# Kernel tuning notes

Measured on AMD Instinct MI355X. Metric: run time of the kernel, lower is better.

## Reference

```python
import jax, jax.numpy as jnp
import numpy as np

B, S, H, DH = 4, 1024, 8, 64
D = H * DH
CLIP_K = 5
NUM_RPR = 2 * CLIP_K + 1  # 11


def setup_inputs() -> dict:
    key = jax.random.key(0)
    ks = jax.random.split(key, 12)
    w_scale = 0.01  # truncated_normal stddev approx
    inp = {
        'q': jax.random.normal(ks[0], (B, S, D), jnp.float32),
        'k': jax.random.normal(ks[1], (B, S, D), jnp.float32),
        'v': jax.random.normal(ks[2], (B, S, D), jnp.float32),
        'rpr_matrix': jax.random.randint(ks[3], (S, S), 0, NUM_RPR, jnp.int32),
        'wq_kernel': jax.random.normal(ks[4], (D, D), jnp.float32) * w_scale,
        'wq_bias': jnp.zeros((D,), jnp.float32),
        'wk_kernel': jax.random.normal(ks[5], (D, D), jnp.float32) * w_scale,
        'wk_bias': jnp.zeros((D,), jnp.float32),
        'wv_kernel': jax.random.normal(ks[6], (D, D), jnp.float32) * w_scale,
        'wv_bias': jnp.zeros((D,), jnp.float32),
        'krpr': jax.random.normal(ks[7], (NUM_RPR, DH), jnp.float32),
    }
    return inp


def reference(q, k, v, rpr_matrix, wq_kernel, wq_bias, wk_kernel, wk_bias,
              wv_kernel, wv_bias, krpr):
    b, s, d = q.shape
    dh = krpr.shape[-1]
    h = d // dh

    def proj(x, w, bias):
        # [B,S,D] -> [B,H,S,DH]
        y = x.reshape(-1, d) @ w + bias
        return y.reshape(b, s, h, dh).transpose(0, 2, 1, 3)

    qh = proj(q, wq_kernel, wq_bias)
    kh = proj(k, wk_kernel, wk_bias)
    vh = proj(v, wv_kernel, wv_bias)

    # standard QK^T scores
    scores = jnp.einsum('bhqd,bhkd->bhqk', qh, kh)
    # RPR key bias: gather per-relative-position key embeddings (note: original
    # code uses krpr for BOTH the key-side and value-side RPR; vrpr is unused)
    alpha = krpr[rpr_matrix]  # [Sq, Sk, DH]
    scores = scores + jnp.einsum('bhqd,qkd->bhqk', qh, alpha)
    scores = scores / jnp.sqrt(jnp.float32(dh))

    probs = jax.nn.softmax(scores, axis=-1)

    ctx = jnp.einsum('bhqk,bhkd->bhqd', probs, vh)
    ctx = ctx + jnp.einsum('bhqk,qkd->bhqd', probs, alpha)

    # [B,H,S,DH] -> [B,S,D]
    return ctx.transpose(0, 2, 1, 3).reshape(b, s, d)
```

## Files before the change

kernel.cpp:

```cpp
#include <hip/hip_runtime.h>

typedef unsigned short u16;
typedef unsigned int u32;
typedef __attribute__((ext_vector_type(8))) short short8;
typedef __attribute__((ext_vector_type(4))) float f32x4;

__device__ __forceinline__ float bf2f(u16 v) {
  return __uint_as_float(((u32)v) << 16);
}
__device__ __forceinline__ u16 f2bf(float f) {
  u32 u = __float_as_uint(f);
  return (u16)((u + 0x7fffu + ((u >> 16) & 1u)) >> 16);
}
__device__ __forceinline__ u32 pk2(float lo, float hi) {
  return (u32)f2bf(lo) | ((u32)f2bf(hi) << 16);
}

__device__ __forceinline__ float ld1in(const void* p, size_t i, bool f32) {
  return f32 ? ((const float*)p)[i] : bf2f(((const u16*)p)[i]);
}
__device__ __forceinline__ float4 ld4in(const void* p, size_t i, bool f32) {
  if (f32) return *(const float4*)((const float*)p + i);
  ushort4 u = *(const ushort4*)((const u16*)p + i);
  return make_float4(bf2f(u.x), bf2f(u.y), bf2f(u.z), bf2f(u.w));
}

__device__ __forceinline__ float4 ld4ws(const u16* p, size_t i) {
  ushort4 u = *(const ushort4*)(p + i);
  return make_float4(bf2f(u.x), bf2f(u.y), bf2f(u.z), bf2f(u.w));
}
__device__ __forceinline__ uint4 ld8ws_pk(const u16* p, size_t i) {
  return *(const uint4*)(p + i);
}


__global__ void rpr_detect_kernel(const u16* __restrict__ q, int* __restrict__ flag) {
  __shared__ int cnt[256];
  int t = threadIdx.x, c = 0;
  for (int i = t; i < 8192; i += 256) {
    unsigned e = (q[i] >> 7) & 0xff;
    c += (e >= 0xC0) ? 1 : 0;
  }
  cnt[t] = c;
  __syncthreads();
  if (t == 0) {
    int s = 0;
    for (int i = 0; i < 256; ++i) s += cnt[i];
    *flag = (s > 128) ? 1 : 0;
  }
}

template <typename WT>
__global__ __launch_bounds__(256, 2) void rpr_proj_mfma(
    const void* __restrict__ xq, const void* __restrict__ xk, const void* __restrict__ xv,
    const void* __restrict__ wqp, const void* __restrict__ wkp, const void* __restrict__ wvp,
    const void* __restrict__ bqp, const void* __restrict__ bkp, const void* __restrict__ bvp,
    WT* __restrict__ ws, const int* __restrict__ flagp) {
  const bool f32 = (*flagp != 0);
  const int z = blockIdx.z;
  const void* __restrict__ X = (z == 0) ? xq : (z == 1) ? xk : xv;
  const void* __restrict__ W = (z == 0) ? wqp : (z == 1) ? wkp : wvp;
  const void* __restrict__ Bb = (z == 0) ? bqp : (z == 1) ? bkp : bvp;
  WT* __restrict__ O = ws + (size_t)z * (4096u * 512u);

  __shared__ u32 as32[2][64][20];
  __shared__ u32 bs32[2][64][20];

  const int t = threadIdx.x;
  const int wvi = t >> 6, lane = t & 63;
  const int quad = lane >> 4, col = lane & 15;
  const int m0 = blockIdx.y * 64, n0 = blockIdx.x * 64;
  const int am = t >> 2, akc = t & 3;
  const int bkx = t & 15, bnx = (t >> 4) * 4;

  f32x4 acc[4] = {{0.f, 0.f, 0.f, 0.f}, {0.f, 0.f, 0.f, 0.f},
                  {0.f, 0.f, 0.f, 0.f}, {0.f, 0.f, 0.f, 0.f}};

  auto loadA = [&](int k0, uint4& ra) {
    if (!f32) {
      ra = *(const uint4*)((const u16*)X + (size_t)(m0 + am) * 512 + k0 + akc * 8);
    } else {
      const float* xf = (const float*)X + (size_t)(m0 + am) * 512 + k0 + akc * 8;
      float4 a = *(const float4*)xf, b = *(const float4*)(xf + 4);
      ra.x = pk2(a.x, a.y); ra.y = pk2(a.z, a.w);
      ra.z = pk2(b.x, b.y); ra.w = pk2(b.z, b.w);
    }
  };
  auto loadB = [&](int k0, uint4& rb) {
    if (!f32) {
      const u16* w0 = (const u16*)W + (size_t)(k0 + 2 * bkx) * 512 + n0 + bnx;
      ushort4 r0 = *(const ushort4*)w0;
      ushort4 r1 = *(const ushort4*)(w0 + 512);
      rb.x = (u32)r0.x | ((u32)r1.x << 16);
      rb.y = (u32)r0.y | ((u32)r1.y << 16);
      rb.z = (u32)r0.z | ((u32)r1.z << 16);
      rb.w = (u32)r0.w | ((u32)r1.w << 16);
    } else {
      float4 r0 = ld4in(W, (size_t)(k0 + 2 * bkx) * 512 + n0 + bnx, true);
      float4 r1 = ld4in(W, (size_t)(k0 + 2 * bkx + 1) * 512 + n0 + bnx, true);
      rb.x = pk2(r0.x, r1.x);
      rb.y = pk2(r0.y, r1.y);
      rb.z = pk2(r0.z, r1.z);
      rb.w = pk2(r0.w, r1.w);
    }
  };

  {
    uint4 ra, rb;
    loadA(0, ra);
    loadB(0, rb);
    *(uint4*)&as32[0][am][akc * 4] = ra;
    bs32[0][bnx + 0][bkx] = rb.x;
    bs32[0][bnx + 1][bkx] = rb.y;
    bs32[0][bnx + 2][bkx] = rb.z;
    bs32[0][bnx + 3][bkx] = rb.w;
  }
  __syncthreads();

  for (int it = 0; it < 16; ++it) {
    const int cur = it & 1;
    uint4 ra, rb;
    if (it < 15) {
      loadA((it + 1) * 32, ra);
      loadB((it + 1) * 32, rb);
    }
    short8 aF = *(const short8*)((const u16*)&as32[cur][wvi * 16 + col][0] + quad * 8);
#pragma unroll
    for (int c = 0; c < 4; ++c) {
      short8 bF = *(const short8*)((const u16*)&bs32[cur][c * 16 + col][0] + quad * 8);
      acc[c] = __builtin_amdgcn_mfma_f32_16x16x32_bf16(aF, bF, acc[c], 0, 0, 0);
    }
    if (it < 15) {
      *(uint4*)&as32[1 - cur][am][akc * 4] = ra;
      bs32[1 - cur][bnx + 0][bkx] = rb.x;
      bs32[1 - cur][bnx + 1][bkx] = rb.y;
      bs32[1 - cur][bnx + 2][bkx] = rb.z;
      bs32[1 - cur][bnx + 3][bkx] = rb.w;
    }
    __syncthreads();
  }

  const int h = blockIdx.x;
#pragma unroll
  for (int c = 0; c < 4; ++c) {
    float bias = ld1in(Bb, (size_t)(n0 + c * 16 + col), f32);
#pragma unroll
    for (int reg = 0; reg < 4; ++reg) {
      int m = m0 + wvi * 16 + quad * 4 + reg;
      int bb = m >> 10, s = m & 1023;
      O[((size_t)((bb * 8 + h) * 1024 + s)) * 64 + c * 16 + col] =
          f2bf(acc[c][reg] + bias);
    }
  }
}

template <typename WT>
__global__ __launch_bounds__(256, 2) void rpr_attn_mfma(
    const WT* __restrict__ qkv, const int* __restrict__ rpr,
    const void* __restrict__ krpr, void* __restrict__ out,
    const int* __restrict__ flagp) {
  const bool f32 = (*flagp != 0);
  const int bh = blockIdx.y, q0 = blockIdx.x * 64;
  const int b = bh >> 3, h = bh & 7;
  const WT* __restrict__ qh = qkv + (size_t)bh * 65536;
  const WT* __restrict__ kh = qkv + (size_t)(32 + bh) * 65536;
  const WT* __restrict__ vh = qkv + (size_t)(64 + bh) * 65536;

  __shared__ u16 qs[64][72];
  __shared__ u16 ks[2][64][72];
  __shared__ u32 vs32[2][64][36];
  __shared__ u16 ps[4][16][72];
  __shared__ float krl[11][64];
  __shared__ float qrpr[64][12];

  const int t = threadIdx.x;
  const int wvi = t >> 6, lane = t & 63;
  const int quad = lane >> 4, col = lane & 15;
  const int sr = t >> 2, sc4 = (t & 3) * 16;
  const int kp = t & 31, dg = (t >> 5) * 8;

  for (int i = t; i < 704; i += 256)
    krl[i >> 6][i & 63] = f32 ? ((const float*)krpr)[i] : bf2f(((const u16*)krpr)[i]);
  {
    size_t base = (size_t)(q0 + sr) * 64 + sc4;
    *(uint4*)&qs[sr][sc4] = ld8ws_pk(qh, base);
    *(uint4*)&qs[sr][sc4 + 8] = ld8ws_pk(qh, base + 8);
  }
  {
    size_t kb = (size_t)sr * 64 + sc4;
    *(uint4*)&ks[0][sr][sc4] = ld8ws_pk(kh, kb);
    *(uint4*)&ks[0][sr][sc4 + 8] = ld8ws_pk(kh, kb + 8);
    size_t vb = (size_t)(2 * kp) * 64 + dg;
    uint4 va = ld8ws_pk(vh, vb), vbb = ld8ws_pk(vh, vb + 64);
    vs32[0][dg + 0][kp] = (va.x & 0xffffu) | (vbb.x << 16);
    vs32[0][dg + 1][kp] = (va.x >> 16) | (vbb.x & 0xffff0000u);
    vs32[0][dg + 2][kp] = (va.y & 0xffffu) | (vbb.y << 16);
    vs32[0][dg + 3][kp] = (va.y >> 16) | (vbb.y & 0xffff0000u);
    vs32[0][dg + 4][kp] = (va.z & 0xffffu) | (vbb.z << 16);
    vs32[0][dg + 5][kp] = (va.z >> 16) | (vbb.z & 0xffff0000u);
    vs32[0][dg + 6][kp] = (va.w & 0xffffu) | (vbb.w << 16);
    vs32[0][dg + 7][kp] = (va.w >> 16) | (vbb.w & 0xffff0000u);
  }
  __syncthreads();
  {
    int r = t >> 2, rb = t & 3;
    float d0 = 0.f, d1 = 0.f, d2 = 0.f;
    for (int d = 0; d < 64; ++d) {
      float qv = bf2f(qs[r][d]);
      d0 = fmaf(qv, krl[rb][d], d0);
      d1 = fmaf(qv, krl[rb + 4][d], d1);
      if (rb < 3) d2 = fmaf(qv, krl[rb + 8][d], d2);
    }
    qrpr[r][rb] = d0;
    qrpr[r][rb + 4] = d1;
    if (rb < 3) qrpr[r][rb + 8] = d2;
  }
  short8 qA0, qA1;
  {
    const u16* qrow = &qs[wvi * 16 + col][0];
    qA0 = *(const short8*)(qrow + quad * 8);
    qA1 = *(const short8*)(qrow + 32 + quad * 8);
  }
  __syncthreads();

  float l_part[4] = {0.f, 0.f, 0.f, 0.f};
  float bins[4][11] = {};
  f32x4 ctx[4] = {{0.f, 0.f, 0.f, 0.f}, {0.f, 0.f, 0.f, 0.f},
                  {0.f, 0.f, 0.f, 0.f}, {0.f, 0.f, 0.f, 0.f}};

  for (int kt = 0; kt < 16; ++kt) {
    const int cur = kt & 1;
    uint4 pk0, pk1, pva, pvb;
    if (kt < 15) {
      size_t kb = (size_t)((kt + 1) * 64 + sr) * 64 + sc4;
      pk0 = ld8ws_pk(kh, kb);
      pk1 = ld8ws_pk(kh, kb + 8);
      size_t vb = (size_t)((kt + 1) * 64 + 2 * kp) * 64 + dg;
      pva = ld8ws_pk(vh, vb);
      pvb = ld8ws_pk(vh, vb + 64);
    }
    int rid[4][4];
    {
      const int* rbase =
          rpr + (size_t)(q0 + wvi * 16 + quad * 4) * 1024 + kt * 64 + col;
#pragma unroll
      for (int reg = 0; reg < 4; ++reg)
#pragma unroll
        for (int c = 0; c < 4; ++c) rid[c][reg] = rbase[reg * 1024 + c * 16];
    }
    f32x4 sc[4];
#pragma unroll
    for (int c = 0; c < 4; ++c) {
      const u16* kb = &ks[cur][c * 16 + col][0];
      short8 kB0 = *(const short8*)(kb + quad * 8);
      short8 kB1 = *(const short8*)(kb + 32 + quad * 8);
      f32x4 a = {0.f, 0.f, 0.f, 0.f};
      a = __builtin_amdgcn_mfma_f32_16x16x32_bf16(qA0, kB0, a, 0, 0, 0);
      a = __builtin_amdgcn_mfma_f32_16x16x32_bf16(qA1, kB1, a, 0, 0, 0);
      sc[c] = a;
    }
#pragma unroll
    for (int c = 0; c < 4; ++c) {
#pragma unroll
      for (int reg = 0; reg < 4; ++reg) {
        int row = wvi * 16 + quad * 4 + reg;
        float p = __expf((sc[c][reg] + qrpr[row][rid[c][reg]]) * 0.125f);
        l_part[reg] += p;
#pragma unroll
        for (int r = 0; r < 11; ++r) bins[reg][r] += (rid[c][reg] == r) ? p : 0.f;
        ps[wvi][quad * 4 + reg][c * 16 + col] = f2bf(p);
      }
    }
    __syncthreads();

    short8 pA0, pA1;
    {
      const u16* prow = &ps[wvi][col][0];
      pA0 = *(const short8*)(prow + quad * 8);
      pA1 = *(const short8*)(prow + 32 + quad * 8);
    }
#pragma unroll
    for (int c = 0; c < 4; ++c) {
      const u16* vrow = (const u16*)&vs32[cur][c * 16 + col][0];
      short8 vB0 = *(const short8*)(vrow + quad * 8);
      short8 vB1 = *(const short8*)(vrow + 32 + quad * 8);
      ctx[c] = __builtin_amdgcn_mfma_f32_16x16x32_bf16(pA0, vB0, ctx[c], 0, 0, 0);
      ctx[c] = __builtin_amdgcn_mfma_f32_16x16x32_bf16(pA1, vB1, ctx[c], 0, 0, 0);
    }
    if (kt < 15) {
      *(uint4*)&ks[1 - cur][sr][sc4] = pk0;
      *(uint4*)&ks[1 - cur][sr][sc4 + 8] = pk1;
      vs32[1 - cur][dg + 0][kp] = (pva.x & 0xffffu) | (pvb.x << 16);
      vs32[1 - cur][dg + 1][kp] = (pva.x >> 16) | (pvb.x & 0xffff0000u);
      vs32[1 - cur][dg + 2][kp] = (pva.y & 0xffffu) | (pvb.y << 16);
      vs32[1 - cur][dg + 3][kp] = (pva.y >> 16) | (pvb.y & 0xffff0000u);
      vs32[1 - cur][dg + 4][kp] = (pva.z & 0xffffu) | (pvb.z << 16);
      vs32[1 - cur][dg + 5][kp] = (pva.z >> 16) | (pvb.z & 0xffff0000u);
      vs32[1 - cur][dg + 6][kp] = (pva.w & 0xffffu) | (pvb.w << 16);
      vs32[1 - cur][dg + 7][kp] = (pva.w >> 16) | (pvb.w & 0xffff0000u);
    }
    __syncthreads();
  }

#pragma unroll
  for (int off = 1; off < 16; off <<= 1) {
#pragma unroll
    for (int reg = 0; reg < 4; ++reg) {
      l_part[reg] += __shfl_xor(l_part[reg], off);
#pragma unroll
      for (int r = 0; r < 11; ++r) bins[reg][r] += __shfl_xor(bins[reg][r], off);
    }
  }
#pragma unroll
  for (int reg = 0; reg < 4; ++reg) {
    int row = wvi * 16 + quad * 4 + reg;
    float inv = 1.f / l_part[reg];
#pragma unroll
    for (int c = 0; c < 4; ++c) {
      float v = ctx[c][reg];
#pragma unroll
      for (int r = 0; r < 11; ++r) v = fmaf(bins[reg][r], krl[r][c * 16 + col], v);
      size_t oidx = (size_t)(b * 1024 + q0 + row) * 512 + h * 64 + c * 16 + col;
      if (f32) ((float*)out)[oidx] = v * inv;
      else ((u16*)out)[oidx] = f2bf(v * inv);
    }
  }
}

extern "C" void kernel_launch(void* const* d_in, const int* in_sizes, int n_in,
                              void* d_out, int out_size, void* d_ws, size_t ws_size,
                              hipStream_t stream) {
  const void* q = d_in[0];
  const void* k = d_in[1];
  const void* v = d_in[2];
  const int* rpr = (const int*)d_in[3];
  const void* wq = d_in[4];
  const void* bq = d_in[5];
  const void* wk = d_in[6];
  const void* bk = d_in[7];
  const void* wv = d_in[8];
  const void* bv = d_in[9];
  const void* krpr = d_in[10];

  int* flag = (int*)d_ws;
  u16* ws = (u16*)((char*)d_ws + 1024);

  rpr_detect_kernel<<<1, 256, 0, stream>>>((const u16*)q, flag);
  rpr_proj_mfma<u16><<<dim3(8, 64, 3), 256, 0, stream>>>(
      q, k, v, wq, wk, wv, bq, bk, bv, ws, flag);
  rpr_attn_mfma<u16><<<dim3(16, 32), 256, 0, stream>>>(
      ws, rpr, krpr, d_out, flag);
}
```

Measured before the change: 190.9 us.

## Fold softmax scale into exp2, pack P stores, fdot2 RPR binning, permute V rows

Folds the 1/sqrt(dh)*log2(e) scale into qrpr and uses raw v_exp_f32 with an fma in place of __expf. The RPR-bin accumulation becomes packed f16 fdot2 with bitmask selectors instead of 11 compare-selects per element. P is converted with hardware packed bf16 conversion and stored as 8-byte chunks in a permuted column order, with V rows loaded in a matching permuted order so the PV product still lines up. One __syncthreads after the P store is removed, relying on each wave reading only its own ps slice. The costs are f16 rounding of probabilities inside the bin sums and a dependence on the V/P permutation being exactly consistent.

```diff
diff --git a/kernel.cpp b/kernel.cpp
--- a/kernel.cpp
+++ b/kernel.cpp
@@ -4,6 +4,7 @@
 typedef unsigned int u32;
 typedef __attribute__((ext_vector_type(8))) short short8;
 typedef __attribute__((ext_vector_type(4))) float f32x4;
+typedef _Float16 f16x2 __attribute__((ext_vector_type(2)));
 
 __device__ __forceinline__ float bf2f(u16 v) {
   return __uint_as_float(((u32)v) << 16);
@@ -169,7 +170,7 @@
   __shared__ u16 qs[64][72];
   __shared__ u16 ks[2][64][72];
   __shared__ u32 vs32[2][64][36];
-  __shared__ u16 ps[4][16][72];
+  __shared__ alignas(16) u16 ps[4][16][72];
   __shared__ float krl[11][64];
   __shared__ float qrpr[64][12];
 
@@ -178,6 +179,7 @@
   const int quad = lane >> 4, col = lane & 15;
   const int sr = t >> 2, sc4 = (t & 3) * 16;
   const int kp = t & 31, dg = (t >> 5) * 8;
+  const int vr0 = (kp & 1) * 32 + (kp >> 1);
 
   for (int i = t; i < 704; i += 256)
     krl[i >> 6][i & 63] = f32 ? ((const float*)krpr)[i] : bf2f(((const u16*)krpr)[i]);
@@ -190,8 +192,8 @@
     size_t kb = (size_t)sr * 64 + sc4;
     *(uint4*)&ks[0][sr][sc4] = ld8ws_pk(kh, kb);
     *(uint4*)&ks[0][sr][sc4 + 8] = ld8ws_pk(kh, kb + 8);
-    size_t vb = (size_t)(2 * kp) * 64 + dg;
-    uint4 va = ld8ws_pk(vh, vb), vbb = ld8ws_pk(vh, vb + 64);
+    size_t vb = (size_t)vr0 * 64 + dg;
+    uint4 va = ld8ws_pk(vh, vb), vbb = ld8ws_pk(vh, vb + 1024);
     vs32[0][dg + 0][kp] = (va.x & 0xffffu) | (vbb.x << 16);
     vs32[0][dg + 1][kp] = (va.x >> 16) | (vbb.x & 0xffff0000u);
     vs32[0][dg + 2][kp] = (va.y & 0xffffu) | (vbb.y << 16);
@@ -203,6 +205,7 @@
   }
   __syncthreads();
   {
+    const float SC = 0.18033688011112042f;
     int r = t >> 2, rb = t & 3;
     float d0 = 0.f, d1 = 0.f, d2 = 0.f;
     for (int d = 0; d < 64; ++d) {
@@ -211,9 +214,9 @@
       d1 = fmaf(qv, krl[rb + 4][d], d1);
       if (rb < 3) d2 = fmaf(qv, krl[rb + 8][d], d2);
     }
-    qrpr[r][rb] = d0;
-    qrpr[r][rb + 4] = d1;
-    if (rb < 3) qrpr[r][rb + 8] = d2;
+    qrpr[r][rb] = d0 * SC;
+    qrpr[r][rb + 4] = d1 * SC;
+    if (rb < 3) qrpr[r][rb + 8] = d2 * SC;
   }
   short8 qA0, qA1;
   {
@@ -235,9 +238,9 @@
       size_t kb = (size_t)((kt + 1) * 64 + sr) * 64 + sc4;
       pk0 = ld8ws_pk(kh, kb);
       pk1 = ld8ws_pk(kh, kb + 8);
-      size_t vb = (size_t)((kt + 1) * 64 + 2 * kp) * 64 + dg;
+      size_t vb = (size_t)((kt + 1) * 64 + vr0) * 64 + dg;
       pva = ld8ws_pk(vh, vb);
-      pvb = ld8ws_pk(vh, vb + 64);
+      pvb = ld8ws_pk(vh, vb + 1024);
     }
     int rid[4][4];
     {
@@ -260,18 +263,43 @@
       sc[c] = a;
     }
 #pragma unroll
-    for (int c = 0; c < 4; ++c) {
-#pragma unroll
-      for (int reg = 0; reg < 4; ++reg) {
-        int row = wvi * 16 + quad * 4 + reg;
-        float p = __expf((sc[c][reg] + qrpr[row][rid[c][reg]]) * 0.125f);
-        l_part[reg] += p;
-#pragma unroll
-        for (int r = 0; r < 11; ++r) bins[reg][r] += (rid[c][reg] == r) ? p : 0.f;
-        ps[wvi][quad * 4 + reg][c * 16 + col] = f2bf(p);
+    for (int reg = 0; reg < 4; ++reg) {
+      const int row = wvi * 16 + quad * 4 + reg;
+      float p4[4];
+#pragma unroll
+      for (int c = 0; c < 4; ++c) {
+        float x = fmaf(sc[c][reg], 0.18033688011112042f, qrpr[row][rid[c][reg]]);
+        float pe;
+        asm("v_exp_f32 %0, %1" : "=v"(pe) : "v"(x));
+        p4[c] = pe;
+        l_part[reg] += pe;
       }
-    }
-    __syncthreads();
+#if __has_builtin(__builtin_amdgcn_fdot2) && __has_builtin(__builtin_amdgcn_cvt_pkrtz)
+      f16x2 ph01 = __builtin_bit_cast(f16x2, __builtin_amdgcn_cvt_pkrtz(p4[0], p4[1]));
+      f16x2 ph23 = __builtin_bit_cast(f16x2, __builtin_amdgcn_cvt_pkrtz(p4[2], p4[3]));
+      u32 m01 = (1u << (u32)rid[0][reg]) | (0x10000u << (u32)rid[1][reg]);
+      u32 m23 = (1u << (u32)rid[2][reg]) | (0x10000u << (u32)rid[3][reg]);
+#pragma unroll
+      for (int r = 0; r < 11; ++r) {
+        u32 s01 = ((m01 >> r) & 0x00010001u) * 0x3C00u;
+        u32 s23 = ((m23 >> r) & 0x00010001u) * 0x3C00u;
+        bins[reg][r] = __builtin_amdgcn_fdot2(ph01, __builtin_bit_cast(f16x2, s01),
+                                              bins[reg][r], false);
+        bins[reg][r] = __builtin_amdgcn_fdot2(ph23, __builtin_bit_cast(f16x2, s23),
+                                              bins[reg][r], false);
+      }
+#else
+#pragma unroll
+      for (int c = 0; c < 4; ++c)
+#pragma unroll
+        for (int r = 0; r < 11; ++r)
+          bins[reg][r] += (rid[c][reg] == r) ? p4[c] : 0.f;
+#endif
+      u32 plo, phi;
+      asm("v_cvt_pk_bf16_f32 %0, %1, %2" : "=v"(plo) : "v"(p4[0]), "v"(p4[1]));
+      asm("v_cvt_pk_bf16_f32 %0, %1, %2" : "=v"(phi) : "v"(p4[2]), "v"(p4[3]));
+      *(uint2*)&ps[wvi][quad * 4 + reg][col * 4] = make_uint2(plo, phi);
+    }
 
     short8 pA0, pA1;
     {
```

Result: faster. 181.5 us (-4.9%).

## Split key tile across two wave groups in attention, with fp16 dot2 binning and exp2

Applied to the files above, without the earlier changes.

The attention block grows to 512 threads, and each of the two wave halves handles 32 of the 64 keys per tile. The partial context, row sums and RPR bins are then merged through shared memory at the end. The softmax scale is folded into an exp2 constant and applied to the precomputed q·krpr table. Per-bin accumulation now uses packed fp16 dot2 with bitmask selectors, and the per-wave P buffer reuses the Q staging area. The aim is more parallelism and less VALU work per key, at the cost of an extra reduction step and lower-precision (fp16 RTZ) bin sums.

```diff
diff --git a/kernel.cpp b/kernel.cpp
--- a/kernel.cpp
+++ b/kernel.cpp
@@ -4,6 +4,7 @@
 typedef unsigned int u32;
 typedef __attribute__((ext_vector_type(8))) short short8;
 typedef __attribute__((ext_vector_type(4))) float f32x4;
+typedef _Float16 f16x2 __attribute__((ext_vector_type(2)));
 
 __device__ __forceinline__ float bf2f(u16 v) {
   return __uint_as_float(((u32)v) << 16);
@@ -25,29 +26,23 @@
   return make_float4(bf2f(u.x), bf2f(u.y), bf2f(u.z), bf2f(u.w));
 }
 
-__device__ __forceinline__ float4 ld4ws(const u16* p, size_t i) {
-  ushort4 u = *(const ushort4*)(p + i);
-  return make_float4(bf2f(u.x), bf2f(u.y), bf2f(u.z), bf2f(u.w));
-}
 __device__ __forceinline__ uint4 ld8ws_pk(const u16* p, size_t i) {
   return *(const uint4*)(p + i);
 }
 
 
 __global__ void rpr_detect_kernel(const u16* __restrict__ q, int* __restrict__ flag) {
-  __shared__ int cnt[256];
+  __shared__ int cnt4[4];
   int t = threadIdx.x, c = 0;
   for (int i = t; i < 8192; i += 256) {
     unsigned e = (q[i] >> 7) & 0xff;
     c += (e >= 0xC0) ? 1 : 0;
   }
-  cnt[t] = c;
-  __syncthreads();
-  if (t == 0) {
-    int s = 0;
-    for (int i = 0; i < 256; ++i) s += cnt[i];
-    *flag = (s > 128) ? 1 : 0;
-  }
+#pragma unroll
+  for (int off = 1; off < 64; off <<= 1) c += __shfl_xor(c, off);
+  if ((t & 63) == 0) cnt4[t >> 6] = c;
+  __syncthreads();
+  if (t == 0) *flag = (cnt4[0] + cnt4[1] + cnt4[2] + cnt4[3] > 128) ? 1 : 0;
 }
 
 template <typename WT>
@@ -155,7 +150,7 @@
 }
 
 template <typename WT>
-__global__ __launch_bounds__(256, 2) void rpr_attn_mfma(
+__global__ __launch_bounds__(512, 4) void rpr_attn_mfma(
     const WT* __restrict__ qkv, const int* __restrict__ rpr,
     const void* __restrict__ krpr, void* __restrict__ out,
     const int* __restrict__ flagp) {
@@ -166,58 +161,51 @@
   const WT* __restrict__ kh = qkv + (size_t)(32 + bh) * 65536;
   const WT* __restrict__ vh = qkv + (size_t)(64 + bh) * 65536;
 
-  __shared__ u16 qs[64][72];
   __shared__ u16 ks[2][64][72];
   __shared__ u32 vs32[2][64][36];
-  __shared__ u16 ps[4][16][72];
+  __shared__ u16 qps[64][72];
   __shared__ float krl[11][64];
   __shared__ float qrpr[64][12];
 
   const int t = threadIdx.x;
-  const int wvi = t >> 6, lane = t & 63;
+  const int w = t >> 6, lane = t & 63;
   const int quad = lane >> 4, col = lane & 15;
-  const int sr = t >> 2, sc4 = (t & 3) * 16;
-  const int kp = t & 31, dg = (t >> 5) * 8;
-
-  for (int i = t; i < 704; i += 256)
+  const int qg = w & 3, h2 = w >> 2;
+  const int sr = t >> 3, sc = (t & 7) * 8;
+  const int kp = t & 31, dgv = (t >> 5) * 4;
+  const int vr0 = (kp & 15) + (kp >> 4) * 32;
+
+  u16* __restrict__ psw = &qps[0][0] + w * (16 * 36);
+
+  for (int i = t; i < 704; i += 512)
     krl[i >> 6][i & 63] = f32 ? ((const float*)krpr)[i] : bf2f(((const u16*)krpr)[i]);
+  *(uint4*)&qps[sr][sc] = ld8ws_pk(qh, (size_t)(q0 + sr) * 64 + sc);
+  *(uint4*)&ks[0][sr][sc] = ld8ws_pk(kh, (size_t)sr * 64 + sc);
   {
-    size_t base = (size_t)(q0 + sr) * 64 + sc4;
-    *(uint4*)&qs[sr][sc4] = ld8ws_pk(qh, base);
-    *(uint4*)&qs[sr][sc4 + 8] = ld8ws_pk(qh, base + 8);
-  }
+    const u16* vp = vh + (size_t)vr0 * 64 + dgv;
+    uint2 va = *(const uint2*)vp;
+    uint2 vbb = *(const uint2*)(vp + 1024);
+    vs32[0][dgv + 0][kp] = (va.x & 0xffffu) | (vbb.x << 16);
+    vs32[0][dgv + 1][kp] = (va.x >> 16) | (vbb.x & 0xffff0000u);
+    vs32[0][dgv + 2][kp] = (va.y & 0xffffu) | (vbb.y << 16);
+    vs32[0][dgv + 3][kp] = (va.y >> 16) | (vbb.y & 0xffff0000u);
+  }
+  __syncthreads();
   {
-    size_t kb = (size_t)sr * 64 + sc4;
-    *(uint4*)&ks[0][sr][sc4] = ld8ws_pk(kh, kb);
-    *(uint4*)&ks[0][sr][sc4 + 8] = ld8ws_pk(kh, kb + 8);
-    size_t vb = (size_t)(2 * kp) * 64 + dg;
-    uint4 va = ld8ws_pk(vh, vb), vbb = ld8ws_pk(vh, vb + 64);
-    vs32[0][dg + 0][kp] = (va.x & 0xffffu) | (vbb.x << 16);
-    vs32[0][dg + 1][kp] = (va.x >> 16) | (vbb.x & 0xffff0000u);
-    vs32[0][dg + 2][kp] = (va.y & 0xffffu) | (vbb.y << 16);
-    vs32[0][dg + 3][kp] = (va.y >> 16) | (vbb.y & 0xffff0000u);
-    vs32[0][dg + 4][kp] = (va.z & 0xffffu) | (vbb.z << 16);
-    vs32[0][dg + 5][kp] = (va.z >> 16) | (vbb.z & 0xffff0000u);
-    vs32[0][dg + 6][kp] = (va.w & 0xffffu) | (vbb.w << 16);
-    vs32[0][dg + 7][kp] = (va.w >> 16) | (vbb.w & 0xffff0000u);
-  }
-  __syncthreads();
-  {
-    int r = t >> 2, rb = t & 3;
-    float d0 = 0.f, d1 = 0.f, d2 = 0.f;
+    const float SC = 0.18033688011112042f;
+    int r = t >> 3, j = t & 7;
+    float d0 = 0.f, d1 = 0.f;
     for (int d = 0; d < 64; ++d) {
-      float qv = bf2f(qs[r][d]);
-      d0 = fmaf(qv, krl[rb][d], d0);
-      d1 = fmaf(qv, krl[rb + 4][d], d1);
-      if (rb < 3) d2 = fmaf(qv, krl[rb + 8][d], d2);
-    }
-    qrpr[r][rb] = d0;
-    qrpr[r][rb + 4] = d1;
-    if (rb < 3) qrpr[r][rb + 8] = d2;
+      float qv = bf2f(qps[r][d]);
+      d0 = fmaf(qv, krl[j][d], d0);
+      if (j < 3) d1 = fmaf(qv, krl[j + 8][d], d1);
+    }
+    qrpr[r][j] = d0 * SC;
+    if (j < 3) qrpr[r][j + 8] = d1 * SC;
   }
   short8 qA0, qA1;
   {
-    const u16* qrow = &qs[wvi * 16 + col][0];
+    const u16* qrow = &qps[qg * 16 + col][0];
     qA0 = *(const short8*)(qrow + quad * 8);
     qA1 = *(const short8*)(qrow + 32 + quad * 8);
   }
@@ -230,99 +218,129 @@
 
   for (int kt = 0; kt < 16; ++kt) {
     const int cur = kt & 1;
-    uint4 pk0, pk1, pva, pvb;
+    uint4 pk;
+    uint2 pva, pvb;
     if (kt < 15) {
-      size_t kb = (size_t)((kt + 1) * 64 + sr) * 64 + sc4;
-      pk0 = ld8ws_pk(kh, kb);
-      pk1 = ld8ws_pk(kh, kb + 8);
-      size_t vb = (size_t)((kt + 1) * 64 + 2 * kp) * 64 + dg;
-      pva = ld8ws_pk(vh, vb);
-      pvb = ld8ws_pk(vh, vb + 64);
-    }
-    int rid[4][4];
+      pk = ld8ws_pk(kh, (size_t)((kt + 1) * 64 + sr) * 64 + sc);
+      const u16* vp = vh + (size_t)((kt + 1) * 64 + vr0) * 64 + dgv;
+      pva = *(const uint2*)vp;
+      pvb = *(const uint2*)(vp + 1024);
+    }
+    int rid[2][4];
     {
       const int* rbase =
-          rpr + (size_t)(q0 + wvi * 16 + quad * 4) * 1024 + kt * 64 + col;
+          rpr + (size_t)(q0 + qg * 16 + quad * 4) * 1024 + kt * 64 + h2 * 32 + col;
 #pragma unroll
       for (int reg = 0; reg < 4; ++reg)
 #pragma unroll
-        for (int c = 0; c < 4; ++c) rid[c][reg] = rbase[reg * 1024 + c * 16];
-    }
-    f32x4 sc[4];
-#pragma unroll
-    for (int c = 0; c < 4; ++c) {
-      const u16* kb = &ks[cur][c * 16 + col][0];
+        for (int c = 0; c < 2; ++c) rid[c][reg] = rbase[reg * 1024 + c * 16];
+    }
+    f32x4 sc2[2];
+#pragma unroll
+    for (int c = 0; c < 2; ++c) {
+      const u16* kb = &ks[cur][(2 * h2 + c) * 16 + col][0];
       short8 kB0 = *(const short8*)(kb + quad * 8);
       short8 kB1 = *(const short8*)(kb + 32 + quad * 8);
       f32x4 a = {0.f, 0.f, 0.f, 0.f};
       a = __builtin_amdgcn_mfma_f32_16x16x32_bf16(qA0, kB0, a, 0, 0, 0);
       a = __builtin_amdgcn_mfma_f32_16x16x32_bf16(qA1, kB1, a, 0, 0, 0);
-      sc[c] = a;
-    }
+      sc2[c] = a;
+    }
+#pragma unroll
+    for (int reg = 0; reg < 4; ++reg) {
+      const int row = qg * 16 + quad * 4 + reg;
+      float p2[2];
+#pragma unroll
+      for (int c = 0; c < 2; ++c) {
+        float x = fmaf(sc2[c][reg], 0.18033688011112042f, qrpr[row][rid[c][reg]]);
+        float pe;
+        asm("v_exp_f32 %0, %1" : "=v"(pe) : "v"(x));
+        p2[c] = pe;
+        l_part[reg] += pe;
+      }
+      f16x2 ph = __builtin_bit_cast(f16x2, __builtin_amdgcn_cvt_pkrtz(p2[0], p2[1]));
+      u32 m01 = (1u << (u32)rid[0][reg]) | (0x10000u << (u32)rid[1][reg]);
+#pragma unroll
+      for (int r = 0; r < 11; ++r) {
+        u32 s01 = ((m01 >> r) & 0x00010001u) * 0x3C00u;
+        bins[reg][r] = __builtin_amdgcn_fdot2(ph, __builtin_bit_cast(f16x2, s01),
+                                              bins[reg][r], false);
+      }
+      u32 pw;
+      asm("v_cvt_pk_bf16_f32 %0, %1, %2" : "=v"(pw) : "v"(p2[0]), "v"(p2[1]));
+      *(u32*)(psw + (quad * 4 + reg) * 36 + col * 2) = pw;
+    }
+
+    short8 pA = *(const short8*)(psw + col * 36 + quad * 8);
 #pragma unroll
     for (int c = 0; c < 4; ++c) {
+      const u16* vrow = (const u16*)&vs32[cur][c * 16 + col][0] + h2 * 32 + quad * 8;
+      short8 vB = *(const short8*)vrow;
+      ctx[c] = __builtin_amdgcn_mfma_f32_16x16x32_bf16(pA, vB, ctx[c], 0, 0, 0);
+    }
+    if (kt < 15) {
+      *(uint4*)&ks[1 - cur][sr][sc] = pk;
+      vs32[1 - cur][dgv + 0][kp] = (pva.x & 0xffffu) | (pvb.x << 16);
+      vs32[1 - cur][dgv + 1][kp] = (pva.x >> 16) | (pvb.x & 0xffff0000u);
+      vs32[1 - cur][dgv + 2][kp] = (pva.y & 0xffffu) | (pvb.y << 16);
+      vs32[1 - cur][dgv + 3][kp] = (pva.y >> 16) | (pvb.y & 0xffff0000u);
+    }
+    __syncthreads();
+  }
+
+#pragma unroll
+  for (int off = 1; off < 16; off <<= 1) {
+#pragma unroll
+    for (int reg = 0; reg < 4; ++reg) {
+      l_part[reg] += __shfl_xor(l_part[reg], off);
+#pragma unroll
+      for (int r = 0; r < 11; ++r) bins[reg][r] += __shfl_xor(bins[reg][r], off);
+    }
+  }
+
+  float* __restrict__ cm = (float*)&ks[0][0][0];
+  float* __restrict__ lb = (float*)&vs32[0][0][0];
+  if (h2 == 1) {
+    float* cp = cm + ((size_t)(qg * 64 + lane)) * 16;
+#pragma unroll
+    for (int c = 0; c < 4; ++c)
+#pragma unroll
+      for (int reg = 0; reg < 4; ++reg) cp[c * 4 + reg] = ctx[c][reg];
+    if (col == 0) {
+      float* lp = lb + (size_t)((qg * 4 + quad) * 4) * 12;
 #pragma unroll
       for (int reg = 0; reg < 4; ++reg) {
-        int row = wvi * 16 + quad * 4 + reg;
-        float p = __expf((sc[c][reg] + qrpr[row][rid[c][reg]]) * 0.125f);
-        l_part[reg] += p;
-#pragma unroll
-        for (int r = 0; r < 11; ++r) bins[reg][r] += (rid[c][reg] == r) ? p : 0.f;
-        ps[wvi][quad * 4 + reg][c * 16 + col] = f2bf(p);
+        lp[reg * 12] = l_part[reg];
+#pragma unroll
+        for (int r = 0; r < 11; ++r) lp[reg * 12 + 1 + r] = bins[reg][r];
       }
     }
-    __syncthreads();
-
-    short8 pA0, pA1;
-    {
-      const u16* prow = &ps[wvi][col][0];
-      pA0 = *(const short8*)(prow + quad * 8);
-      pA1 = *(const short8*)(prow + 32 + quad * 8);
-    }
-#pragma unroll
-    for (int c = 0; c < 4; ++c) {
-      const u16* vrow = (const u16*)&vs32[cur][c * 16 + col][0];
-      short8 vB0 = *(const short8*)(vrow + quad * 8);
-      short8 vB1 = *(const short8*)(vrow + 32 + quad * 8);
-      ctx[c] = __builtin_amdgcn_mfma_f32_16x16x32_bf16(pA0, vB0, ctx[c], 0, 0, 0);
-      ctx[c] = __builtin_amdgcn_mfma_f32_16x16x32_bf16(pA1, vB1, ctx[c], 0, 0, 0);
-    }
-    if (kt < 15) {
-      *(uint4*)&ks[1 - cur][sr][sc4] = pk0;
-      *(uint4*)&ks[1 - cur][sr][sc4 + 8] = pk1;
-      vs32[1 - cur][dg + 0][kp] = (pva.x & 0xffffu) | (pvb.x << 16);
-      vs32[1 - cur][dg + 1][kp] = (pva.x >> 16) | (pvb.x & 0xffff0000u);
-      vs32[1 - cur][dg + 2][kp] = (pva.y & 0xffffu) | (pvb.y << 16);
-      vs32[1 - cur][dg + 3][kp] = (pva.y >> 16) | (pvb.y & 0xffff0000u);
-      vs32[1 - cur][dg + 4][kp] = (pva.z & 0xffffu) | (pvb.z << 16);
-      vs32[1 - cur][dg + 5][kp] = (pva.z >> 16) | (pvb.z & 0xffff0000u);
-      vs32[1 - cur][dg + 6][kp] = (pva.w & 0xffffu) | (pvb.w << 16);
-      vs32[1 - cur][dg + 7][kp] = (pva.w >> 16) | (pvb.w & 0xffff0000u);
-    }
-    __syncthreads();
-  }
-
-#pragma unroll
-  for (int off = 1; off < 16; off <<= 1) {
-#pragma unroll
-    for (int reg = 0; reg < 4; ++reg) {
-      l_part[reg] += __shfl_xor(l_part[reg], off);
-#pragma unroll
-      for (int r = 0; r < 11; ++r) bins[reg][r] += __shfl_xor(bins[reg][r], off);
-    }
-  }
-#pragma unroll
-  for (int reg = 0; reg < 4; ++reg) {
-    int row = wvi * 16 + quad * 4 + reg;
-    float inv = 1.f / l_part[reg];
-#pragma unroll
-    for (int c = 0; c < 4; ++c) {
-      float v = ctx[c][reg];
-#pragma unroll
-      for (int r = 0; r < 11; ++r) v = fmaf(bins[reg][r], krl[r][c * 16 + col], v);
-      size_t oidx = (size_t)(b * 1024 + q0 + row) * 512 + h * 64 + c * 16 + col;
-      if (f32) ((float*)out)[oidx] = v * inv;
-      else ((u16*)out)[oidx] = f2bf(v * inv);
+  }
+  __syncthreads();
+  if (h2 == 0) {
+    const float* cp = cm + ((size_t)(qg * 64 + lane)) * 16;
+    const float* lp = lb + (size_t)((qg * 4 + quad) * 4) * 12;
+#pragma unroll
+    for (int reg = 0; reg < 4; ++reg) {
+      l_part[reg] += lp[reg * 12];
+#pragma unroll
+      for (int r = 0; r < 11; ++r) bins[reg][r] += lp[reg * 12 + 1 + r];
+#pragma unroll
+      for (int c = 0; c < 4; ++c) ctx[c][reg] += cp[c * 4 + reg];
+    }
+#pragma unroll
+    for (int reg = 0; reg < 4; ++reg) {
+      int row = qg * 16 + quad * 4 + reg;
+      float inv = 1.f / l_part[reg];
+#pragma unroll
+      for (int c = 0; c < 4; ++c) {
+        float v = ctx[c][reg];
+#pragma unroll
+        for (int r = 0; r < 11; ++r) v = fmaf(bins[reg][r], krl[r][c * 16 + col], v);
+        size_t oidx = (size_t)(b * 1024 + q0 + row) * 512 + h * 64 + c * 16 + col;
+        if (f32) ((float*)out)[oidx] = v * inv;
+        else ((u16*)out)[oidx] = f2bf(v * inv);
+      }
     }
   }
 }
@@ -348,6 +366,6 @@
   rpr_detect_kernel<<<1, 256, 0, stream>>>((const u16*)q, flag);
   rpr_proj_mfma<u16><<<dim3(8, 64, 3), 256, 0, stream>>>(
       q, k, v, wq, wk, wv, bq, bk, bv, ws, flag);
-  rpr_attn_mfma<u16><<<dim3(16, 32), 256, 0, stream>>>(
+  rpr_attn_mfma<u16><<<dim3(16, 32), 512, 0, stream>>>(
       ws, rpr, krpr, d_out, flag);
 }
```

Result: slower. 209.7 us (+9.9%).
